# Kernel tuning notes

Hardware: AMD Instinct MI355X
Metric: run time of the kernel (lower is better)

Reference implementation:

```python
import jax, jax.numpy as jnp
import numpy as np

N = 20000
E = 320000
IN_F = 128
HEADS = 8
OUT_F = 32
NEG_SLOPE = 0.2


def setup_inputs() -> dict:
    key = jax.random.key(0)
    k = jax.random.split(key, 8)
    x = jax.random.normal(k[0], (N, IN_F), dtype=jnp.float32)
    edge_index = jax.random.randint(k[1], (2, E), 0, N, dtype=jnp.int32)
    # Linear weights stored torch-style: [out, in]
    scale = 1.0 / np.sqrt(IN_F)
    W = jax.random.normal(k[2], (HEADS * OUT_F, IN_F), dtype=jnp.float32) * scale
    W1 = jax.random.normal(k[3], (HEADS * OUT_F, IN_F), dtype=jnp.float32) * scale
    W2 = jax.random.normal(k[4], (HEADS * OUT_F, IN_F), dtype=jnp.float32) * scale
    att = jax.random.normal(k[5], (1, HEADS, OUT_F), dtype=jnp.float32) * 0.1
    bias = jnp.zeros((HEADS * OUT_F,), dtype=jnp.float32)
    return {"x": x, "edge_index": edge_index, "W": W, "W1": W1, "W2": W2,
            "att": att, "bias": bias}


def reference(x, edge_index, W, W1, W2, att, bias):
    n, heads, out_f = x.shape[0], att.shape[1], att.shape[2]
    src, dst = edge_index[0], edge_index[1]

    # Node projections: [N, H, F]
    h_src = (x @ W1.T).reshape(n, heads, out_f)
    h_dst = (x @ W2.T).reshape(n, heads, out_f)
    values = (x @ W.T).reshape(n, heads, out_f)

    # Edge-wise GATv2 logits: a^T LeakyReLU(W1 h_i + W2 h_j)  -> [E, H]
    att_input = jax.nn.leaky_relu(h_src[src] + h_dst[dst], negative_slope=NEG_SLOPE)
    logits = jnp.einsum('ehf,hf->eh', att_input, att[0])

    # Segment softmax over incoming edges of each dst node (stable).
    seg_max = jax.ops.segment_max(logits, dst, num_segments=n)  # [N, H]
    exp_l = jnp.exp(logits - seg_max[dst])
    denom = jax.ops.segment_sum(exp_l, dst, num_segments=n)     # [N, H]
    weights = exp_l / denom[dst]                                # [E, H]

    # Weighted aggregation of source values into dst nodes.
    weighted = weights[:, :, None] * values[src]                # [E, H, F]
    out = jax.ops.segment_sum(weighted, dst, num_segments=n)    # [N, H, F]

    out = out.reshape(n, heads * out_f) + bias
    return out
```

## Files before the change

### kernel.cpp

```cpp
#include <hip/hip_runtime.h>
#include <math.h>

#define NN 20000
#define EE 320000
#define KF 128
#define HO 256
#define CAP 96

typedef __attribute__((ext_vector_type(8))) short short8;
typedef __attribute__((ext_vector_type(4))) float f32x4;

static __device__ __forceinline__ unsigned short f2bf(float f) {
    union { float f; unsigned u; } v; v.f = f;
    unsigned u = v.u;
    u += 0x7fffu + ((u >> 16) & 1u);
    return (unsigned short)(u >> 16);
}
static __device__ __forceinline__ float bf2f(unsigned short b) {
    union { unsigned u; float f; } v; v.u = ((unsigned)b) << 16;
    return v.f;
}

__global__ __launch_bounds__(256) void prep_kernel(
    const float* __restrict__ x, const float* __restrict__ W0,
    const float* __restrict__ W1, const float* __restrict__ W2,
    unsigned short* __restrict__ xb, unsigned short* __restrict__ wb,
    int* __restrict__ cursor)
{
    const int b = blockIdx.x;
    const int t = threadIdx.x;
    if (b < 96) {
        const int m = b >> 5;
        const float* __restrict__ Wm = (m == 0) ? W0 : (m == 1) ? W1 : W2;
        int idx = (b & 31) * 1024 + t * 4;
        float4 v = *(const float4*)(Wm + idx);
        ushort4 o;
        o.x = f2bf(v.x); o.y = f2bf(v.y); o.z = f2bf(v.z); o.w = f2bf(v.w);
        *(ushort4*)(wb + (size_t)m * 32768 + idx) = o;
    } else if (b < 2596) {
        size_t i = (size_t)(b - 96) * 1024 + t * 4;
        float4 v = *(const float4*)(x + i);
        ushort4 o;
        o.x = f2bf(v.x); o.y = f2bf(v.y); o.z = f2bf(v.z); o.w = f2bf(v.w);
        *(ushort4*)(xb + i) = o;
    } else {
        int i = (b - 2596) * 256 + t;
        if (i < NN) cursor[i] = 0;
    }
}

__global__ void scatter_kernel(const int* __restrict__ ei, int* __restrict__ cursor,
                               int* __restrict__ csr_src) {
    int e = blockIdx.x * blockDim.x + threadIdx.x;
    if (e < EE) {
        int s = ei[e];
        int d = ei[EE + e];
        int pos = atomicAdd(&cursor[d], 1);
        if (pos < CAP) csr_src[d * CAP + pos] = s;
    }
}

__global__ __launch_bounds__(256, 3) void proj_kernel(
    const unsigned short* __restrict__ xb, const unsigned short* __restrict__ wb,
    unsigned short* __restrict__ hv, unsigned short* __restrict__ hdst)
{
    const int m = blockIdx.y;
    const unsigned short* __restrict__ Wm = wb + (size_t)m * 32768;
    unsigned short* __restrict__ dst = (m == 0) ? (hv + 256) : (m == 1) ? hv : hdst;
    const int stride = (m == 2) ? 256 : 512;

    const int w    = threadIdx.x >> 6;
    const int lane = threadIdx.x & 63;
    const int lr   = lane & 15;
    const int q    = lane >> 4;
    const int cb   = w * 64;

    short8 Bf[4][4];
#pragma unroll
    for (int nt = 0; nt < 4; ++nt)
#pragma unroll
        for (int ks = 0; ks < 4; ++ks)
            Bf[nt][ks] = *(const short8*)(Wm + (size_t)(cb + nt * 16 + lr) * KF + ks * 32 + q * 8);

    const int rb = blockIdx.x * 64;

    short8 Af[4];
    {
        const int arow = rb + lr;
#pragma unroll
        for (int ks = 0; ks < 4; ++ks) {
            Af[ks] = (short8){0,0,0,0,0,0,0,0};
            if (arow < NN)
                Af[ks] = *(const short8*)(xb + (size_t)arow * KF + ks * 32 + q * 8);
        }
    }

#pragma unroll
    for (int it = 0; it < 4; ++it) {
        const int r0 = rb + it * 16;

        short8 An[4];
        if (it < 3) {
            const int arow = r0 + 16 + lr;
#pragma unroll
            for (int ks = 0; ks < 4; ++ks) {
                An[ks] = (short8){0,0,0,0,0,0,0,0};
                if (arow < NN)
                    An[ks] = *(const short8*)(xb + (size_t)arow * KF + ks * 32 + q * 8);
            }
        }

        f32x4 acc[4];
#pragma unroll
        for (int nt = 0; nt < 4; ++nt) acc[nt] = (f32x4){0.f, 0.f, 0.f, 0.f};

#pragma unroll
        for (int ks = 0; ks < 4; ++ks)
#pragma unroll
            for (int nt = 0; nt < 4; ++nt)
                acc[nt] = __builtin_amdgcn_mfma_f32_16x16x32_bf16(Af[ks], Bf[nt][ks], acc[nt], 0, 0, 0);

#pragma unroll
        for (int nt = 0; nt < 4; ++nt) {
#pragma unroll
            for (int r = 0; r < 4; ++r) {
                const int row = r0 + q * 4 + r;
                if (row < NN)
                    dst[(size_t)row * stride + cb + nt * 16 + lr] = f2bf(acc[nt][r]);
            }
        }

        if (it < 3) {
#pragma unroll
            for (int ks = 0; ks < 4; ++ks) Af[ks] = An[ks];
        }
    }
}

__global__ __launch_bounds__(128) void gat_kernel(
    const unsigned short* __restrict__ hv, const unsigned short* __restrict__ hdst,
    const float* __restrict__ att, const float* __restrict__ bias,
    const int* __restrict__ cursor, const int* __restrict__ csr_src,
    float* __restrict__ out)
{
    const int w    = threadIdx.x >> 6;
    const int d    = blockIdx.x * 2 + w;
    const int lane = threadIdx.x & 63;
    const int half = lane >> 5;
    const int sub  = lane & 31;
    const int c8   = sub * 8;

    float a[8], hd[8];
    {
        const float4 aa = *(const float4*)(att + c8);
        const float4 ab = *(const float4*)(att + c8 + 4);
        a[0] = aa.x; a[1] = aa.y; a[2] = aa.z; a[3] = aa.w;
        a[4] = ab.x; a[5] = ab.y; a[6] = ab.z; a[7] = ab.w;
        const short8 h8 = *(const short8*)(hdst + (size_t)d * HO + c8);
#pragma unroll
        for (int j = 0; j < 8; ++j) hd[j] = bf2f((unsigned short)h8[j]);
    }

    int deg = cursor[d];
    if (deg > CAP) deg = CAP;

    int sreg = (lane < deg) ? csr_src[d * CAP + lane] : 0;

    float l = 0.f;
    float o[8] = {0.f, 0.f, 0.f, 0.f, 0.f, 0.f, 0.f, 0.f};

#define EDGE_CALC(HS, VS, MASK)                                               \
    {                                                                         \
        float p = 0.f;                                                        \
        _Pragma("unroll")                                                     \
        for (int j = 0; j < 8; ++j) {                                         \
            float z = bf2f((unsigned short)HS[j]) + hd[j];                    \
            z = fmaxf(z, 0.2f * z);                                           \
            p = fmaf(a[j], z, p);                                             \
        }                                                                     \
        p += __shfl_xor(p, 1);                                                \
        p += __shfl_xor(p, 2);                                                \
        const float e = __expf(p) * (MASK);                                   \
        l += e;                                                               \
        _Pragma("unroll")                                                     \
        for (int j = 0; j < 8; ++j)                                           \
            o[j] = fmaf(e, bf2f((unsigned short)VS[j]), o[j]);                \
    }

    const int nfast = (deg < 64) ? deg : 64;
    const int npair = (nfast + 1) >> 1;
    int i = 0;
    for (; i + 2 <= npair; i += 2) {
        const int i0 = 2 * i + half;
        const int i1 = 2 * (i + 1) + half;
        const int s0 = __shfl(sreg, i0);
        const int s1 = __shfl(sreg, i1);
        const unsigned short* p0 = hv + (size_t)s0 * 512 + c8;
        const unsigned short* p1 = hv + (size_t)s1 * 512 + c8;
        const short8 h0 = *(const short8*)p0;
        const short8 v0 = *(const short8*)(p0 + 256);
        const short8 h1 = *(const short8*)p1;
        const short8 v1 = *(const short8*)(p1 + 256);
        const float m0 = (i0 < deg) ? 1.f : 0.f;
        const float m1 = (i1 < deg) ? 1.f : 0.f;
        EDGE_CALC(h0, v0, m0);
        EDGE_CALC(h1, v1, m1);
    }
    for (; i < npair; ++i) {
        const int i0 = 2 * i + half;
        const int s0 = __shfl(sreg, i0);
        const unsigned short* p0 = hv + (size_t)s0 * 512 + c8;
        const short8 h0 = *(const short8*)p0;
        const short8 v0 = *(const short8*)(p0 + 256);
        const float m0 = (i0 < deg) ? 1.f : 0.f;
        EDGE_CALC(h0, v0, m0);
    }
    for (int j = 64; j < deg; ++j) {
        const int s0 = csr_src[d * CAP + j];
        const unsigned short* p0 = hv + (size_t)s0 * 512 + c8;
        const short8 h0 = *(const short8*)p0;
        const short8 v0 = *(const short8*)(p0 + 256);
        const float m0 = (half == 0) ? 1.f : 0.f;
        EDGE_CALC(h0, v0, m0);
    }
#undef EDGE_CALC

    l += __shfl_xor(l, 32);
#pragma unroll
    for (int j = 0; j < 8; ++j) o[j] += __shfl_xor(o[j], 32);

    const float inv = (deg > 0) ? 1.f / l : 0.f;
    const float s0 = half ? o[4] : o[0];
    const float s1 = half ? o[5] : o[1];
    const float s2 = half ? o[6] : o[2];
    const float s3 = half ? o[7] : o[3];
    const float4 bb = *(const float4*)(bias + c8 + half * 4);
    float4 res;
    res.x = s0 * inv + bb.x;
    res.y = s1 * inv + bb.y;
    res.z = s2 * inv + bb.z;
    res.w = s3 * inv + bb.w;
    *(float4*)(out + (size_t)d * HO + c8 + half * 4) = res;
}

extern "C" void kernel_launch(void* const* d_in, const int* in_sizes, int n_in,
                              void* d_out, int out_size, void* d_ws, size_t ws_size,
                              hipStream_t stream) {
    const float* x    = (const float*)d_in[0];
    const int*   ei   = (const int*)d_in[1];
    const float* W0   = (const float*)d_in[2];
    const float* W1   = (const float*)d_in[3];
    const float* W2   = (const float*)d_in[4];
    const float* att  = (const float*)d_in[5];
    const float* bias = (const float*)d_in[6];
    float* out = (float*)d_out;

    char* p = (char*)d_ws;
    unsigned short* hv   = (unsigned short*)p; p += (size_t)NN * 512 * 2;
    unsigned short* hdst = (unsigned short*)p; p += (size_t)NN * HO * 2;
    unsigned short* xb   = (unsigned short*)p; p += (size_t)NN * KF * 2;
    unsigned short* wb   = (unsigned short*)p; p += (size_t)3 * 32768 * 2;
    int* cursor  = (int*)p; p += (size_t)NN * sizeof(int);
    int* csr_src = (int*)p; p += (size_t)NN * CAP * sizeof(int);

    prep_kernel<<<2675, 256, 0, stream>>>(x, W0, W1, W2, xb, wb, cursor);
    scatter_kernel<<<(EE + 255) / 256, 256, 0, stream>>>(ei, cursor, csr_src);
    proj_kernel<<<dim3(313, 3), 256, 0, stream>>>(xb, wb, hv, hdst);
    gat_kernel<<<NN / 2, 128, 0, stream>>>(hv, hdst, att, bias, cursor, csr_src, out);
}
```

Before: 161.7 us.

## Store projections head-major and split GAT aggregation per head across blocks

```diff
diff --git a/kernel.cpp b/kernel.cpp
--- a/kernel.cpp
+++ b/kernel.cpp
@@ -62,12 +62,10 @@
 
 __global__ __launch_bounds__(256, 3) void proj_kernel(
     const unsigned short* __restrict__ xb, const unsigned short* __restrict__ wb,
-    unsigned short* __restrict__ hv, unsigned short* __restrict__ hdst)
+    unsigned short* __restrict__ hvh, unsigned short* __restrict__ hdd)
 {
     const int m = blockIdx.y;
     const unsigned short* __restrict__ Wm = wb + (size_t)m * 32768;
-    unsigned short* __restrict__ dst = (m == 0) ? (hv + 256) : (m == 1) ? hv : hdst;
-    const int stride = (m == 2) ? 256 : 512;
 
     const int w    = threadIdx.x >> 6;
     const int lane = threadIdx.x & 63;
@@ -122,11 +120,19 @@
 
 #pragma unroll
         for (int nt = 0; nt < 4; ++nt) {
+            const int col = cb + nt * 16 + lr;
+            const int h   = col >> 5;
+            const int f   = col & 31;
+            const size_t cbase = (m == 2)
+                ? ((size_t)h * NN) * 32 + f
+                : ((size_t)h * NN) * 64 + f + (m == 0 ? 32 : 0);
+            unsigned short* __restrict__ outp = (m == 2) ? hdd : hvh;
+            const int rowmul = (m == 2) ? 32 : 64;
 #pragma unroll
             for (int r = 0; r < 4; ++r) {
                 const int row = r0 + q * 4 + r;
                 if (row < NN)
-                    dst[(size_t)row * stride + cb + nt * 16 + lr] = f2bf(acc[nt][r]);
+                    outp[cbase + (size_t)row * rowmul] = f2bf(acc[nt][r]);
             }
         }
 
@@ -137,26 +143,32 @@
     }
 }
 
-__global__ __launch_bounds__(128) void gat_kernel(
-    const unsigned short* __restrict__ hv, const unsigned short* __restrict__ hdst,
+__global__ __launch_bounds__(256) void gat_kernel(
+    const unsigned short* __restrict__ hvh, const unsigned short* __restrict__ hdd,
     const float* __restrict__ att, const float* __restrict__ bias,
     const int* __restrict__ cursor, const int* __restrict__ csr_src,
     float* __restrict__ out)
 {
+    const int bx   = blockIdx.x;
+    const int h    = bx & 7;
+    const int grp  = bx >> 3;
     const int w    = threadIdx.x >> 6;
-    const int d    = blockIdx.x * 2 + w;
+    const int d    = grp * 4 + w;
     const int lane = threadIdx.x & 63;
-    const int half = lane >> 5;
-    const int sub  = lane & 31;
-    const int c8   = sub * 8;
-
-    float a[8], hd[8];
+    const int slot = lane >> 3;
+    const int r    = lane & 7;
+    const int f8   = (r & 3) * 8;
+
+    float a[8];
     {
-        const float4 aa = *(const float4*)(att + c8);
-        const float4 ab = *(const float4*)(att + c8 + 4);
+        const float4 aa = *(const float4*)(att + h * 32 + f8);
+        const float4 ab = *(const float4*)(att + h * 32 + f8 + 4);
         a[0] = aa.x; a[1] = aa.y; a[2] = aa.z; a[3] = aa.w;
         a[4] = ab.x; a[5] = ab.y; a[6] = ab.z; a[7] = ab.w;
-        const short8 h8 = *(const short8*)(hdst + (size_t)d * HO + c8);
+    }
+    float hd[8];
+    {
+        const short8 h8 = *(const short8*)(hdd + ((size_t)h * NN + d) * 32 + f8);
 #pragma unroll
         for (int j = 0; j < 8; ++j) hd[j] = bf2f((unsigned short)h8[j]);
     }
@@ -168,79 +180,64 @@
 
     float l = 0.f;
     float o[8] = {0.f, 0.f, 0.f, 0.f, 0.f, 0.f, 0.f, 0.f};
-
-#define EDGE_CALC(HS, VS, MASK)                                               \
+    const size_t hbase = (size_t)h * NN;
+
+#define EDGE_BODY(SVAL, EIDX)                                                 \
     {                                                                         \
-        float p = 0.f;                                                        \
+        const short8 x8 = *(const short8*)(hvh + (hbase + (SVAL)) * 64 + r * 8); \
+        float pp = 0.f;                                                       \
         _Pragma("unroll")                                                     \
         for (int j = 0; j < 8; ++j) {                                         \
-            float z = bf2f((unsigned short)HS[j]) + hd[j];                    \
+            float z = bf2f((unsigned short)x8[j]) + hd[j];                    \
             z = fmaxf(z, 0.2f * z);                                           \
-            p = fmaf(a[j], z, p);                                             \
+            pp = fmaf(a[j], z, pp);                                           \
         }                                                                     \
-        p += __shfl_xor(p, 1);                                                \
-        p += __shfl_xor(p, 2);                                                \
-        const float e = __expf(p) * (MASK);                                   \
+        pp += __shfl_xor(pp, 1);                                              \
+        pp += __shfl_xor(pp, 2);                                              \
+        const float pv = __shfl_xor(pp, 4);    \
+        const float e = ((EIDX) < deg) ? __expf(pv) : 0.f;                    \
         l += e;                                                               \
         _Pragma("unroll")                                                     \
         for (int j = 0; j < 8; ++j)                                           \
-            o[j] = fmaf(e, bf2f((unsigned short)VS[j]), o[j]);                \
-    }
-
-    const int nfast = (deg < 64) ? deg : 64;
-    const int npair = (nfast + 1) >> 1;
-    int i = 0;
-    for (; i + 2 <= npair; i += 2) {
-        const int i0 = 2 * i + half;
-        const int i1 = 2 * (i + 1) + half;
-        const int s0 = __shfl(sreg, i0);
-        const int s1 = __shfl(sreg, i1);
-        const unsigned short* p0 = hv + (size_t)s0 * 512 + c8;
-        const unsigned short* p1 = hv + (size_t)s1 * 512 + c8;
-        const short8 h0 = *(const short8*)p0;
-        const short8 v0 = *(const short8*)(p0 + 256);
-        const short8 h1 = *(const short8*)p1;
-        const short8 v1 = *(const short8*)(p1 + 256);
-        const float m0 = (i0 < deg) ? 1.f : 0.f;
-        const float m1 = (i1 < deg) ? 1.f : 0.f;
-        EDGE_CALC(h0, v0, m0);
-        EDGE_CALC(h1, v1, m1);
-    }
-    for (; i < npair; ++i) {
-        const int i0 = 2 * i + half;
-        const int s0 = __shfl(sreg, i0);
-        const unsigned short* p0 = hv + (size_t)s0 * 512 + c8;
-        const short8 h0 = *(const short8*)p0;
-        const short8 v0 = *(const short8*)(p0 + 256);
-        const float m0 = (i0 < deg) ? 1.f : 0.f;
-        EDGE_CALC(h0, v0, m0);
-    }
-    for (int j = 64; j < deg; ++j) {
-        const int s0 = csr_src[d * CAP + j];
-        const unsigned short* p0 = hv + (size_t)s0 * 512 + c8;
-        const short8 h0 = *(const short8*)p0;
-        const short8 v0 = *(const short8*)(p0 + 256);
-        const float m0 = (half == 0) ? 1.f : 0.f;
-        EDGE_CALC(h0, v0, m0);
-    }
-#undef EDGE_CALC
-
-    l += __shfl_xor(l, 32);
-#pragma unroll
-    for (int j = 0; j < 8; ++j) o[j] += __shfl_xor(o[j], 32);
-
-    const float inv = (deg > 0) ? 1.f / l : 0.f;
-    const float s0 = half ? o[4] : o[0];
-    const float s1 = half ? o[5] : o[1];
-    const float s2 = half ? o[6] : o[2];
-    const float s3 = half ? o[7] : o[3];
-    const float4 bb = *(const float4*)(bias + c8 + half * 4);
-    float4 res;
-    res.x = s0 * inv + bb.x;
-    res.y = s1 * inv + bb.y;
-    res.z = s2 * inv + bb.z;
-    res.w = s3 * inv + bb.w;
-    *(float4*)(out + (size_t)d * HO + c8 + half * 4) = res;
+            o[j] = fmaf(e, bf2f((unsigned short)x8[j]), o[j]);                \
+    }
+
+    const int niter = (deg + 7) >> 3;
+    const int nfast = (niter < 8) ? niter : 8;
+#pragma unroll 2
+    for (int it = 0; it < nfast; ++it) {
+        const int ei = it * 8 + slot;
+        const int s  = __shfl(sreg, ei);
+        EDGE_BODY(s, ei);
+    }
+    for (int it = 8; it < niter; ++it) {
+        const int ei = it * 8 + slot;
+        const int s  = (ei < deg) ? csr_src[d * CAP + ei] : 0;
+        EDGE_BODY(s, ei);
+    }
+#undef EDGE_BODY
+
+    l += __shfl_xor(l, 8); l += __shfl_xor(l, 16); l += __shfl_xor(l, 32);
+#pragma unroll
+    for (int j = 0; j < 8; ++j) {
+        o[j] += __shfl_xor(o[j], 8);
+        o[j] += __shfl_xor(o[j], 16);
+        o[j] += __shfl_xor(o[j], 32);
+    }
+
+    if (r >= 4) {
+        const float inv = (deg > 0) ? 1.f / l : 0.f;
+        const int fb = h * 32 + f8;
+        const float4 b0 = *(const float4*)(bias + fb);
+        const float4 b1 = *(const float4*)(bias + fb + 4);
+        float4 r0, r1;
+        r0.x = o[0] * inv + b0.x; r0.y = o[1] * inv + b0.y;
+        r0.z = o[2] * inv + b0.z; r0.w = o[3] * inv + b0.w;
+        r1.x = o[4] * inv + b1.x; r1.y = o[5] * inv + b1.y;
+        r1.z = o[6] * inv + b1.z; r1.w = o[7] * inv + b1.w;
+        *(float4*)(out + (size_t)d * HO + fb) = r0;
+        *(float4*)(out + (size_t)d * HO + fb + 4) = r1;
+    }
 }
 
 extern "C" void kernel_launch(void* const* d_in, const int* in_sizes, int n_in,
@@ -256,15 +253,15 @@
     float* out = (float*)d_out;
 
     char* p = (char*)d_ws;
-    unsigned short* hv   = (unsigned short*)p; p += (size_t)NN * 512 * 2;
-    unsigned short* hdst = (unsigned short*)p; p += (size_t)NN * HO * 2;
-    unsigned short* xb   = (unsigned short*)p; p += (size_t)NN * KF * 2;
-    unsigned short* wb   = (unsigned short*)p; p += (size_t)3 * 32768 * 2;
+    unsigned short* hvh = (unsigned short*)p; p += (size_t)8 * NN * 64 * 2;
+    unsigned short* hdd = (unsigned short*)p; p += (size_t)8 * NN * 32 * 2;
+    unsigned short* xb  = (unsigned short*)p; p += (size_t)NN * KF * 2;
+    unsigned short* wb  = (unsigned short*)p; p += (size_t)3 * 32768 * 2;
     int* cursor  = (int*)p; p += (size_t)NN * sizeof(int);
     int* csr_src = (int*)p; p += (size_t)NN * CAP * sizeof(int);
 
     prep_kernel<<<2675, 256, 0, stream>>>(x, W0, W1, W2, xb, wb, cursor);
     scatter_kernel<<<(EE + 255) / 256, 256, 0, stream>>>(ei, cursor, csr_src);
-    proj_kernel<<<dim3(313, 3), 256, 0, stream>>>(xb, wb, hv, hdst);
-    gat_kernel<<<NN / 2, 128, 0, stream>>>(hv, hdst, att, bias, cursor, csr_src, out);
-}
+    proj_kernel<<<dim3(313, 3), 256, 0, stream>>>(xb, wb, hvh, hdd);
+    gat_kernel<<<8 * (NN / 4), 256, 0, stream>>>(hvh, hdd, att, bias, cursor, csr_src, out);
+}
```

After: 196.1 us. +21.3%, slower.
